# Kernel tuning notes

Measured on AMD Instinct MI355X. Metric: run time of the kernel, lower is better.

Reference implementation:

```python
import jax, jax.numpy as jnp
import numpy as np

N = 200000      # total nodes
D = 256         # input_dim
H = 256         # hidden_dim
O = 256         # output_dim
G = 1024        # n_graphs


def setup_inputs() -> dict:
    key = jax.random.key(0)
    ks = jax.random.split(key, 8)
    w = lambda k, shp, fan: jax.random.normal(k, shp, jnp.float32) / np.sqrt(fan)
    # evenly partitioned, sorted segment ids -> every graph non-empty
    batch = ((jnp.arange(N) * G) // N).astype(jnp.int32)
    return {
        "node_features": jax.random.normal(ks[0], (N, D), jnp.float32),
        "batch": batch,
        "num_segments": G,
        "W1": w(ks[1], (D, H), D), "b1": jnp.zeros((H,), jnp.float32),
        "W2": w(ks[2], (H, H), H), "b2": jnp.zeros((H,), jnp.float32),
        "W3": w(ks[3], (H, O), H), "b3": jnp.zeros((O,), jnp.float32),
        "aW1": w(ks[4], (D, H), D), "ab1": jnp.zeros((H,), jnp.float32),
        "aW2": w(ks[5], (H, 1), H), "ab2": jnp.zeros((1,), jnp.float32),
    }


def reference(node_features, batch, num_segments,
              W1, b1, W2, b2, W3, b3, aW1, ab1, aW2, ab2):
    silu = jax.nn.silu
    # MLP: Linear -> SiLU -> Linear -> SiLU -> Linear
    h = silu(node_features @ W1 + b1)
    h = silu(h @ W2 + b2)
    x = h @ W3 + b3                      # (N, O)
    # attention logits: Linear -> SiLU -> Linear(->1)
    logits = (silu(node_features @ aW1 + ab1) @ aW2 + ab2)[:, 0]  # (N,)
    # per-segment stable softmax via segment max/sum
    m = jax.ops.segment_max(logits, batch, num_segments=num_segments)
    ew = jnp.exp(logits - m[batch])
    denom = jax.ops.segment_sum(ew, batch, num_segments=num_segments)
    weights = ew / denom[batch]          # (N,)
    # weighted segment sum -> (G, O)
    out = jax.ops.segment_sum(x * weights[:, None], batch, num_segments=num_segments)
    return out
```

## Files before the change

kernel.cpp:

```cpp
#include <hip/hip_runtime.h>

#define N_NODES 200000
#define DIM 256
#define G_SEG 1024
#define MT 128
#define LDA 264
#define NT 8
#define KSTEPS 8

typedef __bf16 bf16x8 __attribute__((ext_vector_type(8)));
typedef float f32x4 __attribute__((ext_vector_type(4)));
typedef unsigned short us16_t __attribute__((ext_vector_type(16)));
typedef unsigned short us8_t __attribute__((ext_vector_type(8)));
typedef unsigned short us4_t __attribute__((ext_vector_type(4)));

__device__ __forceinline__ unsigned short f2bf(float f) {
  unsigned int u = __float_as_uint(f);
  u = u + 0x7FFFu + ((u >> 16) & 1u);
  return (unsigned short)(u >> 16);
}

__device__ __forceinline__ bf16x8 ld_frag(const unsigned short* p) {
  us8_t r = *(const us8_t*)p;
  return __builtin_bit_cast(bf16x8, r);
}

__device__ __forceinline__ float silu(float v) {
  return v * __builtin_amdgcn_rcpf(1.f + __expf(-v));
}

__device__ __forceinline__ void stage_x(const float* __restrict__ X,
                                        unsigned short* A, int base, int tid) {
  #pragma unroll 4
  for (int i = 0; i < 32; ++i) {
    int flat = i * 256 + tid;
    int row = flat >> 6;
    int c4 = flat & 63;
    int grow = base + row;
    float4 v = make_float4(0.f, 0.f, 0.f, 0.f);
    if (grow < N_NODES) v = *(const float4*)(X + (size_t)grow * DIM + c4 * 4);
    us4_t h;
    h[0] = f2bf(v.x); h[1] = f2bf(v.y); h[2] = f2bf(v.z); h[3] = f2bf(v.w);
    *(us4_t*)(A + row * LDA + c4 * 4) = h;
  }
}

__device__ __forceinline__ void gemm_k256_T(const unsigned short* __restrict__ Wb,
                                            const unsigned short* A,
                                            f32x4 acc[NT][4],
                                            int wcol0, int quad, int l15) {
  for (int ks = 0; ks < KSTEPS; ++ks) {
    int koff = ks * 32 + quad * 8;
    bf16x8 wfr[4];
    #pragma unroll
    for (int u = 0; u < 4; ++u)
      wfr[u] = ld_frag(Wb + (size_t)(wcol0 + u * 16 + l15) * 256 + koff);
    #pragma unroll
    for (int t = 0; t < NT; ++t) {
      bf16x8 xfr = ld_frag(A + (t * 16 + l15) * LDA + koff);
      #pragma unroll
      for (int u = 0; u < 4; ++u)
        acc[t][u] = __builtin_amdgcn_mfma_f32_16x16x32_bf16(wfr[u], xfr, acc[t][u], 0, 0, 0);
    }
  }
}

__device__ __forceinline__ void zero_acc(f32x4 acc[NT][4]) {
  #pragma unroll
  for (int t = 0; t < NT; ++t)
    #pragma unroll
    for (int u = 0; u < 4; ++u)
      acc[t][u] = (f32x4){0.f, 0.f, 0.f, 0.f};
}

__global__ __launch_bounds__(256) void k_prep(
    const float* __restrict__ W1, const float* __restrict__ W2,
    const float* __restrict__ W3, const float* __restrict__ aW1,
    unsigned short* __restrict__ Wb1, unsigned short* __restrict__ Wb2,
    unsigned short* __restrict__ Wb3, unsigned short* __restrict__ aWb1,
    float* __restrict__ out, float* __restrict__ denom) {
  __shared__ float tlds[64][257];
  int b = blockIdx.x, tid = threadIdx.x;
  if (b < 1024) {
    out[b * 256 + tid] = 0.f;
    return;
  }
  if (b == 1024) {
    #pragma unroll
    for (int i = 0; i < 4; ++i) denom[tid * 4 + i] = 0.f;
    return;
  }
  int bb = b - 1025;
  int mat = bb >> 2, kc = bb & 3, k0 = kc * 64;
  const float* W = (mat == 0) ? W1 : (mat == 1) ? W2 : (mat == 2) ? W3 : aW1;
  unsigned short* Wb = (mat == 0) ? Wb1 : (mat == 1) ? Wb2 : (mat == 2) ? Wb3 : aWb1;
  #pragma unroll 8
  for (int i = 0; i < 64; ++i)
    tlds[i][tid] = W[(size_t)(k0 + i) * 256 + tid];
  __syncthreads();
  #pragma unroll
  for (int rep = 0; rep < 4; ++rep) {
    int flat = rep * 256 + tid;
    int n = flat >> 2, c = flat & 3;
    us16_t v;
    #pragma unroll
    for (int j = 0; j < 16; ++j) v[j] = f2bf(tlds[c * 16 + j][n]);
    *(us16_t*)(Wb + (size_t)n * 256 + k0 + c * 16) = v;
  }
}

__global__ __launch_bounds__(256, 2) void k_fused(
    const float* __restrict__ X, const int* __restrict__ batch,
    const unsigned short* __restrict__ aWb1, const float* __restrict__ ab1,
    const float* __restrict__ aW2, const float* __restrict__ ab2,
    const unsigned short* __restrict__ Wb1, const float* __restrict__ b1,
    const unsigned short* __restrict__ Wb2, const float* __restrict__ b2,
    const unsigned short* __restrict__ Wb3, const float* __restrict__ b3,
    float* __restrict__ out, float* __restrict__ denom) {
  __shared__ unsigned short a_lds[MT * LDA];
  __shared__ float l_lds[MT];
  __shared__ float ew0[MT], ew1[MT];
  __shared__ float seg_lds[2];
  int tid = threadIdx.x;
  int base = blockIdx.x * MT;
  stage_x(X, a_lds, base, tid);
  if (tid < MT) l_lds[tid] = 0.f;
  if (tid < 2) seg_lds[tid] = 0.f;
  __syncthreads();

  int wave = tid >> 6, lane = tid & 63, quad = lane >> 4, l15 = lane & 15;
  int wcol0 = wave * 64;
  int fq = wcol0 + quad * 4;
  f32x4 acc[NT][4];

  zero_acc(acc);
  gemm_k256_T(aWb1, a_lds, acc, wcol0, quad, l15);
  {
    float4 ab1c[4], aw2c[4];
    #pragma unroll
    for (int u = 0; u < 4; ++u) {
      ab1c[u] = *(const float4*)(ab1 + fq + u * 16);
      aw2c[u] = *(const float4*)(aW2 + fq + u * 16);
    }
    #pragma unroll
    for (int t = 0; t < NT; ++t) {
      float p = 0.f;
      #pragma unroll
      for (int u = 0; u < 4; ++u) {
        const float* bb = (const float*)&ab1c[u];
        const float* ww = (const float*)&aw2c[u];
        #pragma unroll
        for (int r = 0; r < 4; ++r)
          p += silu(acc[t][u][r] + bb[r]) * ww[r];
      }
      p += __shfl_xor(p, 16); p += __shfl_xor(p, 32);
      if (quad == 0) atomicAdd(&l_lds[t * 16 + l15], p);
    }
  }

  zero_acc(acc);
  gemm_k256_T(Wb1, a_lds, acc, wcol0, quad, l15);
  __syncthreads();
  if (tid < MT) {
    int grow = base + tid;
    float e = 0.f; int ds = 0;
    if (grow < N_NODES) {
      e = __expf(l_lds[tid] + ab2[0]);
      ds = batch[grow] - batch[base];
    }
    ew0[tid] = ds ? 0.f : e;
    ew1[tid] = ds ? e : 0.f;
    if (e != 0.f) atomicAdd(&seg_lds[ds], e);
  }
  {
    float4 bc[4];
    #pragma unroll
    for (int u = 0; u < 4; ++u) bc[u] = *(const float4*)(b1 + fq + u * 16);
    #pragma unroll
    for (int t = 0; t < NT; ++t)
      #pragma unroll
      for (int u = 0; u < 4; ++u) {
        const float* bb = (const float*)&bc[u];
        us4_t h;
        #pragma unroll
        for (int r = 0; r < 4; ++r)
          h[r] = f2bf(silu(acc[t][u][r] + bb[r]));
        *(us4_t*)(a_lds + (t * 16 + l15) * LDA + fq + u * 16) = h;
      }
  }
  __syncthreads();

  zero_acc(acc);
  gemm_k256_T(Wb2, a_lds, acc, wcol0, quad, l15);
  __syncthreads();
  {
    float4 bc[4];
    #pragma unroll
    for (int u = 0; u < 4; ++u) bc[u] = *(const float4*)(b2 + fq + u * 16);
    #pragma unroll
    for (int t = 0; t < NT; ++t)
      #pragma unroll
      for (int u = 0; u < 4; ++u) {
        const float* bb = (const float*)&bc[u];
        us4_t h;
        #pragma unroll
        for (int r = 0; r < 4; ++r)
          h[r] = f2bf(silu(acc[t][u][r] + bb[r]));
        *(us4_t*)(a_lds + (t * 16 + l15) * LDA + fq + u * 16) = h;
      }
  }
  __syncthreads();

  zero_acc(acc);
  gemm_k256_T(Wb3, a_lds, acc, wcol0, quad, l15);
  {
    float4 bc[4];
    #pragma unroll
    for (int u = 0; u < 4; ++u) bc[u] = *(const float4*)(b3 + fq + u * 16);
    float s0a[4][4], s1a[4][4];
    #pragma unroll
    for (int u = 0; u < 4; ++u)
      #pragma unroll
      for (int r = 0; r < 4; ++r) { s0a[u][r] = 0.f; s1a[u][r] = 0.f; }
    #pragma unroll
    for (int t = 0; t < NT; ++t) {
      float w0 = ew0[t * 16 + l15];
      float w1 = ew1[t * 16 + l15];
      #pragma unroll
      for (int u = 0; u < 4; ++u) {
        const float* bb = (const float*)&bc[u];
        #pragma unroll
        for (int r = 0; r < 4; ++r) {
          float x = acc[t][u][r] + bb[r];
          s0a[u][r] += x * w0;
          s1a[u][r] += x * w1;
        }
      }
    }
    int s0 = batch[base];
    #pragma unroll
    for (int u = 0; u < 4; ++u)
      #pragma unroll
      for (int r = 0; r < 4; ++r) {
        float a0 = s0a[u][r];
        a0 += __shfl_xor(a0, 1); a0 += __shfl_xor(a0, 2);
        a0 += __shfl_xor(a0, 4); a0 += __shfl_xor(a0, 8);
        float a1 = s1a[u][r];
        a1 += __shfl_xor(a1, 1); a1 += __shfl_xor(a1, 2);
        a1 += __shfl_xor(a1, 4); a1 += __shfl_xor(a1, 8);
        if (l15 == 0) {
          int col = fq + u * 16 + r;
          atomicAdd(&out[(size_t)s0 * 256 + col], a0);
          if (s0 + 1 < G_SEG && a1 != 0.f)
            atomicAdd(&out[(size_t)(s0 + 1) * 256 + col], a1);
        }
      }
    if (tid < 2) {
      float v = seg_lds[tid];
      if (v != 0.f) atomicAdd(&denom[s0 + tid], v);
    }
  }
}

__global__ __launch_bounds__(256) void k_final(float* __restrict__ out,
                                               const float* __restrict__ denom) {
  int b = blockIdx.x, tid = threadIdx.x;
  float d = denom[b];
  out[b * 256 + tid] *= __builtin_amdgcn_rcpf(d) * (d * __builtin_amdgcn_rcpf(d) > 0.f ? 1.f : 1.f);
}

extern "C" void kernel_launch(void* const* d_in, const int* in_sizes, int n_in,
                              void* d_out, int out_size, void* d_ws, size_t ws_size,
                              hipStream_t stream) {
  const float* X    = (const float*)d_in[0];
  const int* batch  = (const int*)d_in[1];
  const float* W1  = (const float*)d_in[3];
  const float* b1  = (const float*)d_in[4];
  const float* W2  = (const float*)d_in[5];
  const float* b2  = (const float*)d_in[6];
  const float* W3  = (const float*)d_in[7];
  const float* b3  = (const float*)d_in[8];
  const float* aW1 = (const float*)d_in[9];
  const float* ab1 = (const float*)d_in[10];
  const float* aW2 = (const float*)d_in[11];
  const float* ab2 = (const float*)d_in[12];
  float* out = (float*)d_out;

  char* ws = (char*)d_ws;
  unsigned short* Wb1  = (unsigned short*)(ws);
  unsigned short* Wb2  = (unsigned short*)(ws + 131072);
  unsigned short* Wb3  = (unsigned short*)(ws + 262144);
  unsigned short* aWb1 = (unsigned short*)(ws + 393216);
  float* denom = (float*)(ws + 524288);

  hipLaunchKernelGGL(k_prep, dim3(1041), dim3(256), 0, stream,
                     W1, W2, W3, aW1, Wb1, Wb2, Wb3, aWb1, out, denom);
  int nblk = (N_NODES + MT - 1) / MT;
  hipLaunchKernelGGL(k_fused, dim3(nblk), dim3(256), 0, stream,
                     X, batch, aWb1, ab1, aW2, ab2,
                     Wb1, b1, Wb2, b2, Wb3, b3, out, denom);
  hipLaunchKernelGGL(k_final, dim3(G_SEG), dim3(256), 0, stream, out, denom);
}
```

Before: 472.8 us.

## Pool before final linear layer, applying W3 to normalized segment sums

Because the last linear layer is affine and the softmax weights sum to one per segment, the change pools the second hidden activations per segment and applies W3 and b3 once per graph in the final kernel. This removes the third per-node GEMM and one LDS writeback and barrier round from the fused kernel. The final kernel now runs a small FP32 matmul over 1024 graphs. Smaller changes alongside: the LDS row padding is changed from 264 to 260, bf16 packing uses the paired conversion intrinsic, and the attention-logit shared-memory atomics are replaced by per-wave partial sums.

Measured after the change: 522.8 us. 10.6% more time.

```diff
diff --git a/kernel.cpp b/kernel.cpp
--- a/kernel.cpp
+++ b/kernel.cpp
@@ -1,10 +1,11 @@
 #include <hip/hip_runtime.h>
+#include <hip/hip_bf16.h>
 
 #define N_NODES 200000
 #define DIM 256
 #define G_SEG 1024
 #define MT 128
-#define LDA 264
+#define LDA 260
 #define NT 8
 #define KSTEPS 8
 
@@ -12,7 +13,11 @@
 typedef float f32x4 __attribute__((ext_vector_type(4)));
 typedef unsigned short us16_t __attribute__((ext_vector_type(16)));
 typedef unsigned short us8_t __attribute__((ext_vector_type(8)));
-typedef unsigned short us4_t __attribute__((ext_vector_type(4)));
+
+__device__ __forceinline__ unsigned int pack2(float a, float b) {
+  __hip_bfloat162 t = __float22bfloat162_rn(make_float2(a, b));
+  unsigned int r; __builtin_memcpy(&r, &t, 4); return r;
+}
 
 __device__ __forceinline__ unsigned short f2bf(float f) {
   unsigned int u = __float_as_uint(f);
@@ -31,17 +36,16 @@
 
 __device__ __forceinline__ void stage_x(const float* __restrict__ X,
                                         unsigned short* A, int base, int tid) {
-  #pragma unroll 4
-  for (int i = 0; i < 32; ++i) {
+  #pragma unroll 8
+  for (int i = 0; i < MT / 4; ++i) {
     int flat = i * 256 + tid;
     int row = flat >> 6;
     int c4 = flat & 63;
     int grow = base + row;
     float4 v = make_float4(0.f, 0.f, 0.f, 0.f);
     if (grow < N_NODES) v = *(const float4*)(X + (size_t)grow * DIM + c4 * 4);
-    us4_t h;
-    h[0] = f2bf(v.x); h[1] = f2bf(v.y); h[2] = f2bf(v.z); h[3] = f2bf(v.w);
-    *(us4_t*)(A + row * LDA + c4 * 4) = h;
+    uint2 h = make_uint2(pack2(v.x, v.y), pack2(v.z, v.w));
+    *(uint2*)(A + row * LDA + c4 * 4) = h;
   }
 }
 
@@ -75,25 +79,25 @@
 
 __global__ __launch_bounds__(256) void k_prep(
     const float* __restrict__ W1, const float* __restrict__ W2,
-    const float* __restrict__ W3, const float* __restrict__ aW1,
+    const float* __restrict__ aW1,
     unsigned short* __restrict__ Wb1, unsigned short* __restrict__ Wb2,
-    unsigned short* __restrict__ Wb3, unsigned short* __restrict__ aWb1,
-    float* __restrict__ out, float* __restrict__ denom) {
+    unsigned short* __restrict__ aWb1,
+    float* __restrict__ z, float* __restrict__ denom) {
   __shared__ float tlds[64][257];
   int b = blockIdx.x, tid = threadIdx.x;
-  if (b < 1024) {
-    out[b * 256 + tid] = 0.f;
+  if (b < 256) {
+    ((float4*)z)[b * 256 + tid] = make_float4(0.f, 0.f, 0.f, 0.f);
     return;
   }
-  if (b == 1024) {
+  if (b == 256) {
     #pragma unroll
     for (int i = 0; i < 4; ++i) denom[tid * 4 + i] = 0.f;
     return;
   }
-  int bb = b - 1025;
+  int bb = b - 257;
   int mat = bb >> 2, kc = bb & 3, k0 = kc * 64;
-  const float* W = (mat == 0) ? W1 : (mat == 1) ? W2 : (mat == 2) ? W3 : aW1;
-  unsigned short* Wb = (mat == 0) ? Wb1 : (mat == 1) ? Wb2 : (mat == 2) ? Wb3 : aWb1;
+  const float* W = (mat == 0) ? W1 : (mat == 1) ? W2 : aW1;
+  unsigned short* Wb = (mat == 0) ? Wb1 : (mat == 1) ? Wb2 : aWb1;
   #pragma unroll 8
   for (int i = 0; i < 64; ++i)
     tlds[i][tid] = W[(size_t)(k0 + i) * 256 + tid];
@@ -115,16 +119,14 @@
     const float* __restrict__ aW2, const float* __restrict__ ab2,
     const unsigned short* __restrict__ Wb1, const float* __restrict__ b1,
     const unsigned short* __restrict__ Wb2, const float* __restrict__ b2,
-    const unsigned short* __restrict__ Wb3, const float* __restrict__ b3,
-    float* __restrict__ out, float* __restrict__ denom) {
+    float* __restrict__ z, float* __restrict__ denom) {
   __shared__ unsigned short a_lds[MT * LDA];
-  __shared__ float l_lds[MT];
+  __shared__ float l_part[4][MT];
   __shared__ float ew0[MT], ew1[MT];
   __shared__ float seg_lds[2];
   int tid = threadIdx.x;
   int base = blockIdx.x * MT;
   stage_x(X, a_lds, base, tid);
-  if (tid < MT) l_lds[tid] = 0.f;
   if (tid < 2) seg_lds[tid] = 0.f;
   __syncthreads();
 
@@ -154,7 +156,7 @@
           p += silu(acc[t][u][r] + bb[r]) * ww[r];
       }
       p += __shfl_xor(p, 16); p += __shfl_xor(p, 32);
-      if (quad == 0) atomicAdd(&l_lds[t * 16 + l15], p);
+      if (quad == 0) l_part[wave][t * 16 + l15] = p;
     }
   }
 
@@ -165,7 +167,7 @@
     int grow = base + tid;
     float e = 0.f; int ds = 0;
     if (grow < N_NODES) {
-      e = __expf(l_lds[tid] + ab2[0]);
+      e = __expf(l_part[0][tid] + l_part[1][tid] + l_part[2][tid] + l_part[3][tid] + ab2[0]);
       ds = batch[grow] - batch[base];
     }
     ew0[tid] = ds ? 0.f : e;
@@ -181,42 +183,20 @@
       #pragma unroll
       for (int u = 0; u < 4; ++u) {
         const float* bb = (const float*)&bc[u];
-        us4_t h;
-        #pragma unroll
-        for (int r = 0; r < 4; ++r)
-          h[r] = f2bf(silu(acc[t][u][r] + bb[r]));
-        *(us4_t*)(a_lds + (t * 16 + l15) * LDA + fq + u * 16) = h;
+        uint2 h = make_uint2(
+            pack2(silu(acc[t][u][0] + bb[0]), silu(acc[t][u][1] + bb[1])),
+            pack2(silu(acc[t][u][2] + bb[2]), silu(acc[t][u][3] + bb[3])));
+        *(uint2*)(a_lds + (t * 16 + l15) * LDA + fq + u * 16) = h;
       }
   }
   __syncthreads();
 
   zero_acc(acc);
   gemm_k256_T(Wb2, a_lds, acc, wcol0, quad, l15);
-  __syncthreads();
   {
     float4 bc[4];
     #pragma unroll
     for (int u = 0; u < 4; ++u) bc[u] = *(const float4*)(b2 + fq + u * 16);
-    #pragma unroll
-    for (int t = 0; t < NT; ++t)
-      #pragma unroll
-      for (int u = 0; u < 4; ++u) {
-        const float* bb = (const float*)&bc[u];
-        us4_t h;
-        #pragma unroll
-        for (int r = 0; r < 4; ++r)
-          h[r] = f2bf(silu(acc[t][u][r] + bb[r]));
-        *(us4_t*)(a_lds + (t * 16 + l15) * LDA + fq + u * 16) = h;
-      }
-  }
-  __syncthreads();
-
-  zero_acc(acc);
-  gemm_k256_T(Wb3, a_lds, acc, wcol0, quad, l15);
-  {
-    float4 bc[4];
-    #pragma unroll
-    for (int u = 0; u < 4; ++u) bc[u] = *(const float4*)(b3 + fq + u * 16);
     float s0a[4][4], s1a[4][4];
     #pragma unroll
     for (int u = 0; u < 4; ++u)
@@ -231,9 +211,9 @@
         const float* bb = (const float*)&bc[u];
         #pragma unroll
         for (int r = 0; r < 4; ++r) {
-          float x = acc[t][u][r] + bb[r];
-          s0a[u][r] += x * w0;
-          s1a[u][r] += x * w1;
+          float h2 = silu(acc[t][u][r] + bb[r]);
+          s0a[u][r] += h2 * w0;
+          s1a[u][r] += h2 * w1;
         }
       }
     }
@@ -250,9 +230,9 @@
         a1 += __shfl_xor(a1, 4); a1 += __shfl_xor(a1, 8);
         if (l15 == 0) {
           int col = fq + u * 16 + r;
-          atomicAdd(&out[(size_t)s0 * 256 + col], a0);
+          atomicAdd(&z[(size_t)s0 * 256 + col], a0);
           if (s0 + 1 < G_SEG && a1 != 0.f)
-            atomicAdd(&out[(size_t)(s0 + 1) * 256 + col], a1);
+            atomicAdd(&z[(size_t)(s0 + 1) * 256 + col], a1);
         }
       }
     if (tid < 2) {
@@ -262,11 +242,29 @@
   }
 }
 
-__global__ __launch_bounds__(256) void k_final(float* __restrict__ out,
-                                               const float* __restrict__ denom) {
-  int b = blockIdx.x, tid = threadIdx.x;
-  float d = denom[b];
-  out[b * 256 + tid] *= __builtin_amdgcn_rcpf(d) * (d * __builtin_amdgcn_rcpf(d) > 0.f ? 1.f : 1.f);
+__global__ __launch_bounds__(256) void k_final(
+    const float* __restrict__ z, const float* __restrict__ denom,
+    const float* __restrict__ W3, const float* __restrict__ b3,
+    float* __restrict__ out) {
+  __shared__ float zn[8][256];
+  int tid = threadIdx.x;
+  int s0 = blockIdx.x * 8;
+  #pragma unroll
+  for (int i = 0; i < 8; ++i)
+    zn[i][tid] = z[(size_t)(s0 + i) * 256 + tid] / denom[s0 + i];
+  __syncthreads();
+  float o[8];
+  #pragma unroll
+  for (int i = 0; i < 8; ++i) o[i] = 0.f;
+  for (int k = 0; k < 256; ++k) {
+    float w = W3[(size_t)k * 256 + tid];
+    #pragma unroll
+    for (int i = 0; i < 8; ++i) o[i] += zn[i][k] * w;
+  }
+  float bb = b3[tid];
+  #pragma unroll
+  for (int i = 0; i < 8; ++i)
+    out[(size_t)(s0 + i) * 256 + tid] = o[i] + bb;
 }
 
 extern "C" void kernel_launch(void* const* d_in, const int* in_sizes, int n_in,
@@ -289,15 +287,16 @@
   char* ws = (char*)d_ws;
   unsigned short* Wb1  = (unsigned short*)(ws);
   unsigned short* Wb2  = (unsigned short*)(ws + 131072);
-  unsigned short* Wb3  = (unsigned short*)(ws + 262144);
-  unsigned short* aWb1 = (unsigned short*)(ws + 393216);
-  float* denom = (float*)(ws + 524288);
-
-  hipLaunchKernelGGL(k_prep, dim3(1041), dim3(256), 0, stream,
-                     W1, W2, W3, aW1, Wb1, Wb2, Wb3, aWb1, out, denom);
+  unsigned short* aWb1 = (unsigned short*)(ws + 262144);
+  float* z     = (float*)(ws + 393216);
+  float* denom = (float*)(ws + 393216 + 1048576);
+
+  hipLaunchKernelGGL(k_prep, dim3(269), dim3(256), 0, stream,
+                     W1, W2, aW1, Wb1, Wb2, aWb1, z, denom);
   int nblk = (N_NODES + MT - 1) / MT;
   hipLaunchKernelGGL(k_fused, dim3(nblk), dim3(256), 0, stream,
                      X, batch, aWb1, ab1, aW2, ab2,
-                     Wb1, b1, Wb2, b2, Wb3, b3, out, denom);
-  hipLaunchKernelGGL(k_final, dim3(G_SEG), dim3(256), 0, stream, out, denom);
-}
+                     Wb1, b1, Wb2, b2, z, denom);
+  hipLaunchKernelGGL(k_final, dim3(G_SEG / 8), dim3(256), 0, stream,
+                     z, denom, W3, b3, out);
+}
```
